# Optimization experiments

Hardware: AMD Instinct MI355X
Metric: run time of the kernel (lower is better)

The kernel has to match this reference:

```python
import jax, jax.numpy as jnp
import numpy as np

B, S, D, L, H = 8, 1024, 512, 6, 8
HD = D // H


def setup_inputs() -> dict:
    key = jax.random.key(0)
    sc = D ** -0.5
    inp = {
        "xr": jax.random.normal(jax.random.fold_in(key, 0), (B, S, D), jnp.float32),
        "xi": jax.random.normal(jax.random.fold_in(key, 1), (B, S, D), jnp.float32),
    }
    wnames = ["Wq_r", "Wq_i", "Wk_r", "Wk_i", "Wv_r", "Wv_i", "Wo_r", "Wo_i",
              "W1_r", "W1_i", "W2_r", "W2_i"]
    for i, n in enumerate(wnames):
        inp[n] = jax.random.normal(jax.random.fold_in(key, 10 + i), (L, D, D), jnp.float32) * sc
    for n in ["bq_r", "bq_i", "bk_r", "bk_i", "bv_r", "bv_i", "bo_r", "bo_i",
              "b1_r", "b1_i", "b2_r", "b2_i"]:
        inp[n] = jnp.zeros((L, D), jnp.float32)
    g0 = 1.0 / np.sqrt(2.0)  # standard complex-LN affine init
    for n in ["ln1_grr", "ln1_gii", "ln2_grr", "ln2_gii"]:
        inp[n] = jnp.full((L, D), g0, jnp.float32)
    for n in ["ln1_gri", "ln1_br", "ln1_bi", "ln2_gri", "ln2_br", "ln2_bi"]:
        inp[n] = jnp.zeros((L, D), jnp.float32)
    return inp


def clin(xr, xi, Wr, Wi, br, bi):
    # ComplexLinear: (xr + i xi)(Wr + i Wi)^T + (br + i bi)
    yr = xr @ Wr.T - xi @ Wi.T + br
    yi = xr @ Wi.T + xi @ Wr.T + bi
    return yr, yi


def cln(xr, xi, grr, gri, gii, br, bi, eps=1e-5):
    # Complex LayerNorm: 2x2 covariance whitening over the feature dim + affine
    mr = xr.mean(-1, keepdims=True)
    mi = xi.mean(-1, keepdims=True)
    cr, ci = xr - mr, xi - mi
    Vrr = (cr * cr).mean(-1, keepdims=True) + eps
    Vii = (ci * ci).mean(-1, keepdims=True) + eps
    Vri = (cr * ci).mean(-1, keepdims=True)
    s = jnp.sqrt(Vrr * Vii - Vri * Vri)
    t = jnp.sqrt(Vrr + Vii + 2.0 * s)
    st = s * t
    Wrr = (Vii + s) / st
    Wii = (Vrr + s) / st
    Wri = -Vri / st
    hr = Wrr * cr + Wri * ci
    hi = Wri * cr + Wii * ci
    return grr * hr + gri * hi + br, gri * hr + gii * hi + bi


def reference(xr, xi,
              Wq_r, Wq_i, bq_r, bq_i, Wk_r, Wk_i, bk_r, bk_i,
              Wv_r, Wv_i, bv_r, bv_i, Wo_r, Wo_i, bo_r, bo_i,
              W1_r, W1_i, b1_r, b1_i, W2_r, W2_i, b2_r, b2_i,
              ln1_grr, ln1_gri, ln1_gii, ln1_br, ln1_bi,
              ln2_grr, ln2_gri, ln2_gii, ln2_br, ln2_bi):
    b, s, d = xr.shape
    nl = Wq_r.shape[0]
    h = H
    hd = d // h
    scale = hd ** -0.5
    for l in range(nl):
        rr, ri = xr, xi
        qr, qi = clin(xr, xi, Wq_r[l], Wq_i[l], bq_r[l], bq_i[l])
        kr, ki = clin(xr, xi, Wk_r[l], Wk_i[l], bk_r[l], bk_i[l])
        vr, vi = clin(xr, xi, Wv_r[l], Wv_i[l], bv_r[l], bv_i[l])
        split = lambda a: a.reshape(b, s, h, hd)
        qr, qi, kr, ki, vr, vi = map(split, (qr, qi, kr, ki, vr, vi))
        # sm_variante='real': softmax over Re(q k^H) = qr.kr + qi.ki
        logits = (jnp.einsum('bqhd,bkhd->bhqk', qr, kr)
                  + jnp.einsum('bqhd,bkhd->bhqk', qi, ki)) * scale
        A = jax.nn.softmax(logits, axis=-1)  # real-valued attention weights
        o_r = jnp.einsum('bhqk,bkhd->bqhd', A, vr).reshape(b, s, d)
        o_i = jnp.einsum('bhqk,bkhd->bqhd', A, vi).reshape(b, s, d)
        o_r, o_i = clin(o_r, o_i, Wo_r[l], Wo_i[l], bo_r[l], bo_i[l])
        xr, xi = o_r + rr, o_i + ri
        xr, xi = cln(xr, xi, ln1_grr[l], ln1_gri[l], ln1_gii[l], ln1_br[l], ln1_bi[l])
        rr, ri = xr, xi
        hr, hi = clin(xr, xi, W1_r[l], W1_i[l], b1_r[l], b1_i[l])
        hr, hi = jax.nn.relu(hr), jax.nn.relu(hi)  # CReLU; dropout = identity (eval)
        hr, hi = clin(hr, hi, W2_r[l], W2_i[l], b2_r[l], b2_i[l])
        xr, xi = hr + rr, hi + ri
        xr, xi = cln(xr, xi, ln2_grr[l], ln2_gri[l], ln2_gii[l], ln2_br[l], ln2_bi[l])
    return jnp.stack([xr, xi])  # [2, B, S, D] (real, imag)
```

## Files before the change

kernel.cpp:

```cpp
#include <hip/hip_runtime.h>
#include <cstddef>
#include <cstdint>

constexpr int NB   = 8;
constexpr int SEQ  = 1024;
constexpr int DIM  = 512;
constexpr int NL   = 6;
constexpr int NH   = 8;
constexpr int HDIM = 64;
constexpr int ROWS = NB * SEQ;
constexpr size_t BSD = (size_t)ROWS * DIM;
constexpr int KHAT = 1024;

typedef __attribute__((ext_vector_type(8))) short bfrag;
typedef __attribute__((ext_vector_type(4))) float f32x4;
typedef __attribute__((ext_vector_type(4))) unsigned short us4;

__device__ __forceinline__ void f4a(const float4 v, float* a) {
    a[0] = v.x; a[1] = v.y; a[2] = v.z; a[3] = v.w;
}
__device__ __forceinline__ float4 a4f(const float* a) {
    float4 v; v.x = a[0]; v.y = a[1]; v.z = a[2]; v.w = a[3]; return v;
}
__device__ __forceinline__ unsigned short f2bf(float f) {
    union { float f; uint32_t u; } x{f};
    return (unsigned short)((x.u + 0x7fffu + ((x.u >> 16) & 1u)) >> 16);
}
__device__ __forceinline__ float bf2f(unsigned short u) {
    union { uint32_t u; float f; } x;
    x.u = (uint32_t)u << 16;
    return x.f;
}
__device__ __forceinline__ uint32_t cvtpk(float lo, float hi) {
    uint32_t r;
    asm("v_cvt_pk_bf16_f32 %0, %1, %2" : "=v"(r) : "v"(lo), "v"(hi));
    return r;
}
__device__ __forceinline__ void gload16(const unsigned short* g, void* l) {
    __builtin_amdgcn_global_load_lds(
        (const __attribute__((address_space(1))) void*)g,
        (__attribute__((address_space(3))) void*)l, 16, 0, 0);
}

constexpr float ATT_SC = 0.125f * 1.44269504f;

struct PrepArgs {
    const float* Wr[6]; const float* Wi[6];
    const float* br[6]; const float* bi[6];
};

__global__ __launch_bounds__(256)
void prep_kernel(PrepArgs a, unsigned short* __restrict__ Ball,
                 float* __restrict__ biasall, int layer)
{
    const int lin = blockIdx.y;
    const int nh_ = blockIdx.x;
    const float* Wr = a.Wr[lin] + (size_t)layer * DIM * DIM;
    const float* Wi = a.Wi[lin] + (size_t)layer * DIM * DIM;

    bool real; int n0;
    if (lin < 3) { const int dh = nh_ & 127; real = dh < 64; n0 = (nh_ >> 7) * 64 + (dh & 63); }
    else         { real = nh_ < 512; n0 = nh_ & 511; }

    const int t = threadIdx.x;
    const int kk = (t * 4) & 511;
    const bool fh = t < 128;
    const float* src;
    float sgn = 1.f;
    if (fh) src = real ? Wr : Wi;
    else { if (real) { src = Wi; sgn = -1.f; } else src = Wr; }

    float v[4];
    f4a(*(const float4*)(src + (size_t)n0 * 512 + kk), v);
    us4 o;
    #pragma unroll
    for (int j = 0; j < 4; ++j) o[j] = f2bf(sgn * v[j]);
    *(us4*)(Ball + (size_t)lin * KHAT * KHAT + (size_t)nh_ * KHAT + t * 4) = o;
    if (t == 0)
        biasall[lin * KHAT + nh_] = real ? a.br[lin][layer * DIM + n0]
                                         : a.bi[lin][layer * DIM + n0];
}

__global__ __launch_bounds__(256)
void gemm_qkv(const unsigned short* __restrict__ Xh,
              const unsigned short* __restrict__ Ball,
              const float* __restrict__ biasall,
              unsigned short* __restrict__ Qh,
              unsigned short* __restrict__ Kh,
              unsigned short* __restrict__ Vth)
{
    __shared__ __align__(16) unsigned short Asm[2][128 * 32];
    __shared__ __align__(16) unsigned short Bsm[2][128 * 32];

    const int t = threadIdx.x, lane = t & 63, w = t >> 6;
    const int wm = w >> 1, wn = w & 1;
    const int c = lane & 15, g = lane >> 4;

    int bid = blockIdx.y * 24 + blockIdx.x;
    bid = (bid & 7) * 192 + (bid >> 3);
    const int nblk = bid % 24, mblk = bid / 24;
    const int n0g = nblk * 128;
    const int m0 = mblk * 128;
    const int lin = n0g >> 10;
    const int n0 = n0g & 1023;
    const unsigned short* Bh = Ball + (size_t)lin * KHAT * KHAT;
    const float* bias = biasall + lin * KHAT;

    f32x4 acc[4][4];
    #pragma unroll
    for (int i = 0; i < 4; ++i)
        #pragma unroll
        for (int j = 0; j < 4; ++j) acc[i][j] = (f32x4){0.f, 0.f, 0.f, 0.f};

    const int srow = (w << 4) + (lane >> 2);
    const int scol = (lane & 3) * 8;
    const unsigned short* gA0 = Xh + (size_t)(m0 + srow) * KHAT + scol;
    const unsigned short* gA1 = Xh + (size_t)(m0 + 64 + srow) * KHAT + scol;
    const unsigned short* gB0 = Bh + (size_t)(n0 + srow) * KHAT + scol;
    const unsigned short* gB1 = Bh + (size_t)(n0 + 64 + srow) * KHAT + scol;
    char* aB0 = (char*)Asm[0] + (w << 10);
    char* aB1 = (char*)Asm[1] + (w << 10);
    char* bB0 = (char*)Bsm[0] + (w << 10);
    char* bB1 = (char*)Bsm[1] + (w << 10);

    for (int ks = 0; ks < 16; ++ks) {
        const int k0 = ks * 64;
        __syncthreads();
        gload16(gA0 + k0, aB0);
        gload16(gA1 + k0, aB0 + 4096);
        gload16(gB0 + k0, bB0);
        gload16(gB1 + k0, bB0 + 4096);
        gload16(gA0 + k0 + 32, aB1);
        gload16(gA1 + k0 + 32, aB1 + 4096);
        gload16(gB0 + k0 + 32, bB1);
        gload16(gB1 + k0 + 32, bB1 + 4096);
        __syncthreads();

        #pragma unroll
        for (int h = 0; h < 2; ++h) {
            bfrag af[4], bf2[4];
            #pragma unroll
            for (int mi = 0; mi < 4; ++mi)
                af[mi] = *(const bfrag*)(Asm[h] + (wm * 64 + mi * 16 + c) * 32 + g * 8);
            #pragma unroll
            for (int ni = 0; ni < 4; ++ni)
                bf2[ni] = *(const bfrag*)(Bsm[h] + (wn * 64 + ni * 16 + c) * 32 + g * 8);
            #pragma unroll
            for (int mi = 0; mi < 4; ++mi)
                #pragma unroll
                for (int ni = 0; ni < 4; ++ni)
                    acc[mi][ni] = __builtin_amdgcn_mfma_f32_16x16x32_bf16(
                        af[mi], bf2[ni], acc[mi][ni], 0, 0, 0);
        }
    }

    const int mbase = m0 + wm * 64;
    const int nbase = n0 + wn * 64;
    unsigned short* dqk = (lin == 0) ? Qh : Kh;
    #pragma unroll
    for (int mi = 0; mi < 4; ++mi) {
        #pragma unroll
        for (int ni = 0; ni < 4; ++ni) {
            const int n = nbase + ni * 16 + c;
            const float bv = bias[n];
            float v[4];
            #pragma unroll
            for (int r = 0; r < 4; ++r) {
                v[r] = acc[mi][ni][r] + bv;
                if (lin == 0) v[r] *= ATT_SC;
            }
            const int mrow = mbase + mi * 16 + g * 4;
            const int b = mrow >> 10, s = mrow & 1023;
            const int h = n >> 7, dh = n & 127;
            if (lin < 2) {
                const size_t a = ((size_t)(b * NH + h) * SEQ + s) * 128 + dh;
                #pragma unroll
                for (int r = 0; r < 4; ++r) dqk[a + (size_t)r * 128] = f2bf(v[r]);
            } else {
                const int ck = (s & 31) >> 2;
                const int sp = (s & ~31) | ((((ck & 3) << 1) | (ck >> 2)) << 2);
                const size_t a = ((size_t)(b * NH + h) * 128 + dh) * SEQ + sp;
                us4 o;
                #pragma unroll
                for (int r = 0; r < 4; ++r) o[r] = f2bf(v[r]);
                *(us4*)(Vth + a) = o;
            }
        }
    }
}

template <bool RELU>
__global__ __launch_bounds__(256)
void gemm_mfma(const unsigned short* __restrict__ Xh,
               const unsigned short* __restrict__ Bh,
               const float* __restrict__ bias,
               unsigned short* __restrict__ Yh)
{
    __shared__ __align__(16) unsigned short Asm[2][128 * 32];
    __shared__ __align__(16) unsigned short Bsm[2][128 * 32];

    const int t = threadIdx.x, lane = t & 63, w = t >> 6;
    const int wm = w >> 1, wn = w & 1;
    const int c = lane & 15, g = lane >> 4;

    int bid = blockIdx.y * 8 + blockIdx.x;
    bid = (bid & 7) * 64 + (bid >> 3);
    const int n0 = (bid & 7) * 128;
    const int m0 = (bid >> 3) * 128;

    f32x4 acc[4][4];
    #pragma unroll
    for (int i = 0; i < 4; ++i)
        #pragma unroll
        for (int j = 0; j < 4; ++j) acc[i][j] = (f32x4){0.f, 0.f, 0.f, 0.f};

    const int srow = (w << 4) + (lane >> 2);
    const int scol = (lane & 3) * 8;
    const unsigned short* gA0 = Xh + (size_t)(m0 + srow) * KHAT + scol;
    const unsigned short* gA1 = Xh + (size_t)(m0 + 64 + srow) * KHAT + scol;
    const unsigned short* gB0 = Bh + (size_t)(n0 + srow) * KHAT + scol;
    const unsigned short* gB1 = Bh + (size_t)(n0 + 64 + srow) * KHAT + scol;
    char* aB0 = (char*)Asm[0] + (w << 10);
    char* aB1 = (char*)Asm[1] + (w << 10);
    char* bB0 = (char*)Bsm[0] + (w << 10);
    char* bB1 = (char*)Bsm[1] + (w << 10);

    for (int ks = 0; ks < 16; ++ks) {
        const int k0 = ks * 64;
        __syncthreads();
        gload16(gA0 + k0, aB0);
        gload16(gA1 + k0, aB0 + 4096);
        gload16(gB0 + k0, bB0);
        gload16(gB1 + k0, bB0 + 4096);
        gload16(gA0 + k0 + 32, aB1);
        gload16(gA1 + k0 + 32, aB1 + 4096);
        gload16(gB0 + k0 + 32, bB1);
        gload16(gB1 + k0 + 32, bB1 + 4096);
        __syncthreads();

        #pragma unroll
        for (int h = 0; h < 2; ++h) {
            bfrag af[4], bf2[4];
            #pragma unroll
            for (int mi = 0; mi < 4; ++mi)
                af[mi] = *(const bfrag*)(Asm[h] + (wm * 64 + mi * 16 + c) * 32 + g * 8);
            #pragma unroll
            for (int ni = 0; ni < 4; ++ni)
                bf2[ni] = *(const bfrag*)(Bsm[h] + (wn * 64 + ni * 16 + c) * 32 + g * 8);
            #pragma unroll
            for (int mi = 0; mi < 4; ++mi)
                #pragma unroll
                for (int ni = 0; ni < 4; ++ni)
                    acc[mi][ni] = __builtin_amdgcn_mfma_f32_16x16x32_bf16(
                        af[mi], bf2[ni], acc[mi][ni], 0, 0, 0);
        }
    }

    const int mbase = m0 + wm * 64;
    const int nbase = n0 + wn * 64;
    #pragma unroll
    for (int mi = 0; mi < 4; ++mi) {
        #pragma unroll
        for (int ni = 0; ni < 4; ++ni) {
            const int n = nbase + ni * 16 + c;
            const float bv = bias[n];
            const int mrow = mbase + mi * 16 + g * 4;
            #pragma unroll
            for (int r = 0; r < 4; ++r) {
                float v = acc[mi][ni][r] + bv;
                if (RELU) v = fmaxf(v, 0.f);
                Yh[(size_t)(mrow + r) * KHAT + n] = f2bf(v);
            }
        }
    }
}

__global__ __launch_bounds__(256)
void attn_mfma(const unsigned short* __restrict__ Qh,
               const unsigned short* __restrict__ Kh,
               const unsigned short* __restrict__ Vth,
               unsigned short* __restrict__ Ah)
{
    __shared__ __align__(16) char smem[32768];
    char* Ksm = smem;
    char* Vsm = smem + 16384;
    const int t    = threadIdx.x;
    const int lane = t & 63;
    const int wv   = t >> 6;
    const int c    = lane & 15;
    const int g    = lane >> 4;

    int bid = blockIdx.x + 16 * blockIdx.y + 128 * blockIdx.z;
    bid = (bid & 7) * 128 + (bid >> 3);
    const int q0 = (bid & 15) * 64;
    const int bh = bid >> 4;
    const int hh = bh & 7, bb = bh >> 3;
    const size_t qkb = (size_t)bh * SEQ * 128;
    const size_t vtb = (size_t)bh * 128 * SEQ;

    constexpr float THR = 11.0f;

    bfrag qf[4];
    {
        const unsigned short* qp = Qh + qkb + (size_t)(q0 + wv * 16 + c) * 128 + g * 8;
        #pragma unroll
        for (int ks = 0; ks < 4; ++ks) qf[ks] = *(const bfrag*)(qp + ks * 32);
    }

    f32x4 oacc[8];
    #pragma unroll
    for (int i = 0; i < 8; ++i) oacc[i] = (f32x4){0.f, 0.f, 0.f, 0.f};
    float mrun = -1e30f, lrun = 0.f;

    const int kkey = t >> 2, kq = t & 3;
    const unsigned short* kgp = Kh + qkb + (size_t)kkey * 128 + kq * 32;
    const int vd = t >> 1, vh2 = t & 1;
    const unsigned short* vgp = Vth + vtb + (size_t)vd * SEQ + vh2 * 32;

    bfrag krg[4], vrg[4];
    #pragma unroll
    for (int j = 0; j < 4; ++j) krg[j] = *(const bfrag*)(kgp + j * 8);
    #pragma unroll
    for (int j = 0; j < 4; ++j) vrg[j] = *(const bfrag*)(vgp + j * 8);

    for (int k0 = 0; k0 < SEQ; k0 += 64) {
        __syncthreads();
        #pragma unroll
        for (int j = 0; j < 4; ++j) {
            const int boff = (kkey * 256 + (kq * 32 + j * 8) * 2) ^ ((kkey & 7) << 4);
            *(bfrag*)(Ksm + boff) = krg[j];
        }
        #pragma unroll
        for (int j = 0; j < 4; ++j) {
            const int boff = (vd * 128 + (vh2 * 32 + j * 8) * 2) ^ ((vd & 7) << 4);
            *(bfrag*)(Vsm + boff) = vrg[j];
        }
        __syncthreads();

        if (k0 + 64 < SEQ) {
            const int kn = k0 + 64;
            #pragma unroll
            for (int j = 0; j < 4; ++j) krg[j] = *(const bfrag*)(kgp + (size_t)kn * 128 + j * 8);
            #pragma unroll
            for (int j = 0; j < 4; ++j) vrg[j] = *(const bfrag*)(vgp + kn + j * 8);
        }

        f32x4 sa[4];
        #pragma unroll
        for (int nt = 0; nt < 4; ++nt) sa[nt] = (f32x4){0.f, 0.f, 0.f, 0.f};
        __builtin_amdgcn_s_setprio(1);
        #pragma unroll
        for (int nt = 0; nt < 4; ++nt) {
            const int key = nt * 16 + c;
            #pragma unroll
            for (int ks = 0; ks < 4; ++ks) {
                const int boff = (key * 256 + (ks * 32 + g * 8) * 2) ^ ((key & 7) << 4);
                const bfrag bk = *(const bfrag*)(Ksm + boff);
                sa[nt] = __builtin_amdgcn_mfma_f32_16x16x32_bf16(bk, qf[ks], sa[nt], 0, 0, 0);
            }
        }
        __builtin_amdgcn_s_setprio(0);

        float mloc = sa[0][0];
        #pragma unroll
        for (int nt = 0; nt < 4; ++nt)
            #pragma unroll
            for (int r = 0; r < 4; ++r) mloc = fmaxf(mloc, sa[nt][r]);
        if (__any(mloc > mrun + THR)) {
            float mt = mloc;
            mt = fmaxf(mt, __shfl_xor(mt, 16, 64));
            mt = fmaxf(mt, __shfl_xor(mt, 32, 64));
            const float mn = fmaxf(mrun, mt);
            const float fs = exp2f(mrun - mn);
            mrun = mn;
            lrun *= fs;
            #pragma unroll
            for (int i = 0; i < 8; ++i) {
                oacc[i][0] *= fs; oacc[i][1] *= fs; oacc[i][2] *= fs; oacc[i][3] *= fs;
            }
        }

        float p[4][4];
        float psum = 0.f;
        #pragma unroll
        for (int nt = 0; nt < 4; ++nt)
            #pragma unroll
            for (int r = 0; r < 4; ++r) {
                p[nt][r] = exp2f(sa[nt][r] - mrun);
                psum += p[nt][r];
            }
        psum += __shfl_xor(psum, 16, 64);
        psum += __shfl_xor(psum, 32, 64);
        lrun += psum;

        uint32_t pk0[4], pk1[4];
        #pragma unroll
        for (int nt = 0; nt < 4; ++nt) {
            pk0[nt] = cvtpk(p[nt][0], p[nt][1]);
            pk1[nt] = cvtpk(p[nt][2], p[nt][3]);
        }

        __builtin_amdgcn_s_setprio(1);
        #pragma unroll
        for (int k2 = 0; k2 < 2; ++k2) {
            union { uint32_t u[4]; bfrag f; } pb;
            pb.u[0] = pk0[2 * k2];
            pb.u[1] = pk1[2 * k2];
            pb.u[2] = pk0[2 * k2 + 1];
            pb.u[3] = pk1[2 * k2 + 1];
            const int kb2 = (k2 * 32 + g * 8) * 2;
            #pragma unroll
            for (int mtl = 0; mtl < 8; ++mtl) {
                const int d = mtl * 16 + c;
                const bfrag va = *(const bfrag*)(Vsm + ((d * 128 + kb2) ^ ((d & 7) << 4)));
                oacc[mtl] = __builtin_amdgcn_mfma_f32_16x16x32_bf16(va, pb.f, oacc[mtl], 0, 0, 0);
            }
        }
        __builtin_amdgcn_s_setprio(0);
    }

    {
        const float ic = 1.0f / lrun;
        #pragma unroll
        for (int i = 0; i < 8; ++i) {
            oacc[i][0] *= ic; oacc[i][1] *= ic; oacc[i][2] *= ic; oacc[i][3] *= ic;
        }
    }
    __syncthreads();
    float* Ox = (float*)(smem + wv * 8192);
    #pragma unroll
    for (int mtl = 0; mtl < 8; ++mtl)
        #pragma unroll
        for (int r = 0; r < 4; ++r)
            Ox[(mtl * 16 + 4 * g + r) * 16 + c] = oacc[mtl][r];
    asm volatile("s_waitcnt lgkmcnt(0)" ::: "memory");
    __builtin_amdgcn_sched_barrier(0);

    const int q = lane >> 2, qt = lane & 3;
    const int colbase = (qt >> 1) * 512 + hh * 64 + (qt & 1) * 32;
    const size_t rowm = (size_t)bb * SEQ + q0 + wv * 16 + q;
    unsigned short* dst = Ah + rowm * KHAT + colbase;
    #pragma unroll
    for (int j = 0; j < 8; ++j) {
        us4 o;
        #pragma unroll
        for (int e = 0; e < 4; ++e) o[e] = f2bf(Ox[(qt * 32 + j * 4 + e) * 16 + q]);
        *(us4*)(dst + j * 4) = o;
    }
}

__global__ __launch_bounds__(256)
void cln_kernel(const unsigned short* __restrict__ U,
                float* __restrict__ Xr, float* __restrict__ Xi,
                unsigned short* __restrict__ Xh,
                const float* __restrict__ Grr, const float* __restrict__ Gri,
                const float* __restrict__ Gii, const float* __restrict__ Bbr,
                const float* __restrict__ Bbi)
{
    const int lane = threadIdx.x & 63;
    const int row  = blockIdx.x * 4 + (threadIdx.x >> 6);
    const size_t off = (size_t)row * DIM;
    const int c0 = lane * 4;
    const int c1 = 256 + lane * 4;

    float xr[8], xi[8];
    {
        const unsigned short* up = U + (size_t)row * KHAT;
        us4 a0 = *(const us4*)(up + c0);
        us4 a1 = *(const us4*)(up + c1);
        us4 b0 = *(const us4*)(up + 512 + c0);
        us4 b1 = *(const us4*)(up + 512 + c1);
        float t0[4], t1[4];
        f4a(*(const float4*)&Xr[off + c0], t0);
        f4a(*(const float4*)&Xr[off + c1], t1);
        #pragma unroll
        for (int j = 0; j < 4; ++j) { xr[j] = bf2f(a0[j]) + t0[j]; xr[4 + j] = bf2f(a1[j]) + t1[j]; }
        f4a(*(const float4*)&Xi[off + c0], t0);
        f4a(*(const float4*)&Xi[off + c1], t1);
        #pragma unroll
        for (int j = 0; j < 4; ++j) { xi[j] = bf2f(b0[j]) + t0[j]; xi[4 + j] = bf2f(b1[j]) + t1[j]; }
    }

    float sr = 0.f, si = 0.f, srr = 0.f, sii = 0.f, sri = 0.f;
    #pragma unroll
    for (int j = 0; j < 8; ++j) {
        sr += xr[j]; si += xi[j];
        srr = fmaf(xr[j], xr[j], srr);
        sii = fmaf(xi[j], xi[j], sii);
        sri = fmaf(xr[j], xi[j], sri);
    }
    #pragma unroll
    for (int m = 32; m >= 1; m >>= 1) {
        sr  += __shfl_xor(sr,  m, 64);
        si  += __shfl_xor(si,  m, 64);
        srr += __shfl_xor(srr, m, 64);
        sii += __shfl_xor(sii, m, 64);
        sri += __shfl_xor(sri, m, 64);
    }

    const float inv_d = 1.0f / DIM;
    const float mr = sr * inv_d, mi = si * inv_d;
    const float Vrr = srr * inv_d - mr * mr + 1e-5f;
    const float Vii = sii * inv_d - mi * mi + 1e-5f;
    const float Vri = sri * inv_d - mr * mi;
    const float s  = sqrtf(Vrr * Vii - Vri * Vri);
    const float tt = sqrtf(Vrr + Vii + 2.0f * s);
    const float ist = 1.0f / (s * tt);
    const float Wrr = (Vii + s) * ist;
    const float Wii = (Vrr + s) * ist;
    const float Wri = -Vri * ist;

    #pragma unroll
    for (int half = 0; half < 2; ++half) {
        const int c = half ? c1 : c0;
        float grr[4], gri[4], gii[4], pbr[4], pbi[4];
        f4a(*(const float4*)&Grr[c], grr);
        f4a(*(const float4*)&Gri[c], gri);
        f4a(*(const float4*)&Gii[c], gii);
        f4a(*(const float4*)&Bbr[c], pbr);
        f4a(*(const float4*)&Bbi[c], pbi);
        float outr[4], outi[4];
        #pragma unroll
        for (int j = 0; j < 4; ++j) {
            const int idx = half * 4 + j;
            const float cr = xr[idx] - mr;
            const float ci = xi[idx] - mi;
            const float hr = Wrr * cr + Wri * ci;
            const float hi = Wri * cr + Wii * ci;
            outr[j] = fmaf(grr[j], hr, fmaf(gri[j], hi, pbr[j]));
            outi[j] = fmaf(gri[j], hr, fmaf(gii[j], hi, pbi[j]));
        }
        *(float4*)&Xr[off + c] = a4f(outr);
        *(float4*)&Xi[off + c] = a4f(outi);
        us4 hr_, hi_;
        #pragma unroll
        for (int j = 0; j < 4; ++j) { hr_[j] = f2bf(outr[j]); hi_[j] = f2bf(outi[j]); }
        *(us4*)(Xh + (size_t)row * KHAT + c)       = hr_;
        *(us4*)(Xh + (size_t)row * KHAT + 512 + c) = hi_;
    }
}

__global__ __launch_bounds__(256)
void init_cvt(const float* __restrict__ xr, const float* __restrict__ xi,
              float* __restrict__ outr, float* __restrict__ outi,
              unsigned short* __restrict__ Xh)
{
    const size_t i = ((size_t)blockIdx.x * 256 + threadIdx.x) * 4;
    float vr[4], vi[4];
    f4a(*(const float4*)(xr + i), vr);
    f4a(*(const float4*)(xi + i), vi);
    *(float4*)(outr + i) = a4f(vr);
    *(float4*)(outi + i) = a4f(vi);
    const size_t m = i >> 9;
    const int k = (int)(i & 511);
    us4 a, b;
    #pragma unroll
    for (int j = 0; j < 4; ++j) { a[j] = f2bf(vr[j]); b[j] = f2bf(vi[j]); }
    *(us4*)(Xh + m * KHAT + k)       = a;
    *(us4*)(Xh + m * KHAT + 512 + k) = b;
}

extern "C" void kernel_launch(void* const* d_in, const int* in_sizes, int n_in,
                              void* d_out, int out_size, void* d_ws, size_t ws_size,
                              hipStream_t stream) {
    (void)in_sizes; (void)n_in; (void)out_size; (void)ws_size;

    const float* in_xr = (const float*)d_in[0];
    const float* in_xi = (const float*)d_in[1];
    PrepArgs pa;
    pa.Wr[0] = (const float*)d_in[2];  pa.Wi[0] = (const float*)d_in[3];
    pa.Wr[1] = (const float*)d_in[4];  pa.Wi[1] = (const float*)d_in[5];
    pa.Wr[2] = (const float*)d_in[6];  pa.Wi[2] = (const float*)d_in[7];
    pa.Wr[3] = (const float*)d_in[8];  pa.Wi[3] = (const float*)d_in[9];
    pa.Wr[4] = (const float*)d_in[10]; pa.Wi[4] = (const float*)d_in[11];
    pa.Wr[5] = (const float*)d_in[12]; pa.Wi[5] = (const float*)d_in[13];
    pa.br[0] = (const float*)d_in[14]; pa.bi[0] = (const float*)d_in[15];
    pa.br[1] = (const float*)d_in[16]; pa.bi[1] = (const float*)d_in[17];
    pa.br[2] = (const float*)d_in[18]; pa.bi[2] = (const float*)d_in[19];
    pa.br[3] = (const float*)d_in[20]; pa.bi[3] = (const float*)d_in[21];
    pa.br[4] = (const float*)d_in[22]; pa.bi[4] = (const float*)d_in[23];
    pa.br[5] = (const float*)d_in[24]; pa.bi[5] = (const float*)d_in[25];
    const float* ln1_grr = (const float*)d_in[26];
    const float* ln1_gii = (const float*)d_in[27];
    const float* ln2_grr = (const float*)d_in[28];
    const float* ln2_gii = (const float*)d_in[29];
    const float* ln1_gri = (const float*)d_in[30];
    const float* ln1_br  = (const float*)d_in[31];
    const float* ln1_bi  = (const float*)d_in[32];
    const float* ln2_gri = (const float*)d_in[33];
    const float* ln2_br  = (const float*)d_in[34];
    const float* ln2_bi  = (const float*)d_in[35];

    float* outr = (float*)d_out;
    float* outi = outr + BSD;

    char* ws = (char*)d_ws;
    unsigned short* Xh  = (unsigned short*)(ws);
    unsigned short* Qh  = (unsigned short*)(ws + 16777216);
    unsigned short* Kh  = (unsigned short*)(ws + 2 * 16777216);
    unsigned short* Vth = (unsigned short*)(ws + 3 * 16777216);
    unsigned short* Ah  = (unsigned short*)(ws + 4 * 16777216);
    unsigned short* Ball = (unsigned short*)(ws + 5 * 16777216);
    float* biasall = (float*)(ws + 5 * 16777216 + 12582912);
    unsigned short* Uh = Kh;
    unsigned short* Hh = Qh;

    init_cvt<<<ROWS * DIM / 1024, 256, 0, stream>>>(in_xr, in_xi, outr, outi, Xh);

    const dim3 pgrid(KHAT, 6);
    const dim3 qgrid(24, ROWS / 128);
    const dim3 ggrid(KHAT / 128, ROWS / 128);
    const dim3 agrid(SEQ / 64, NH, NB);
    const int  lgrid = ROWS / 4;

    for (int l = 0; l < NL; ++l) {
        const size_t bo = (size_t)l * DIM;
        prep_kernel<<<pgrid, 256, 0, stream>>>(pa, Ball, biasall, l);

        unsigned short* Bo = Ball + (size_t)3 * KHAT * KHAT;
        unsigned short* B1 = Ball + (size_t)4 * KHAT * KHAT;
        unsigned short* B2 = Ball + (size_t)5 * KHAT * KHAT;

        gemm_qkv<<<qgrid, 256, 0, stream>>>(Xh, Ball, biasall, Qh, Kh, Vth);
        attn_mfma<<<agrid, 256, 0, stream>>>(Qh, Kh, Vth, Ah);
        gemm_mfma<false><<<ggrid, 256, 0, stream>>>(Ah, Bo, biasall + 3 * KHAT, Uh);
        cln_kernel<<<lgrid, 256, 0, stream>>>(Uh, outr, outi, Xh,
                                              ln1_grr + bo, ln1_gri + bo, ln1_gii + bo,
                                              ln1_br + bo, ln1_bi + bo);
        gemm_mfma<true><<<ggrid, 256, 0, stream>>>(Xh, B1, biasall + 4 * KHAT, Hh);
        gemm_mfma<false><<<ggrid, 256, 0, stream>>>(Hh, B2, biasall + 5 * KHAT, Uh);
        cln_kernel<<<lgrid, 256, 0, stream>>>(Uh, outr, outi, Xh,
                                              ln2_grr + bo, ln2_gri + bo, ln2_gii + bo,
                                              ln2_br + bo, ln2_bi + bo);
    }
}
```

Before: 1.493 ms.

## Process two query sub-tiles per wave in attention to reuse K/V fragments

```diff
diff --git a/kernel.cpp b/kernel.cpp
--- a/kernel.cpp
+++ b/kernel.cpp
@@ -290,27 +290,30 @@
     const int c    = lane & 15;
     const int g    = lane >> 4;
 
-    int bid = blockIdx.x + 16 * blockIdx.y + 128 * blockIdx.z;
-    bid = (bid & 7) * 128 + (bid >> 3);
-    const int q0 = (bid & 15) * 64;
-    const int bh = bid >> 4;
+    int bid = blockIdx.x + 8 * blockIdx.y + 64 * blockIdx.z;
+    bid = (bid & 7) * 64 + (bid >> 3);
+    const int q0 = (bid & 7) * 128;
+    const int bh = bid >> 3;
     const int hh = bh & 7, bb = bh >> 3;
     const size_t qkb = (size_t)bh * SEQ * 128;
     const size_t vtb = (size_t)bh * 128 * SEQ;
 
     constexpr float THR = 11.0f;
 
-    bfrag qf[4];
-    {
-        const unsigned short* qp = Qh + qkb + (size_t)(q0 + wv * 16 + c) * 128 + g * 8;
-        #pragma unroll
-        for (int ks = 0; ks < 4; ++ks) qf[ks] = *(const bfrag*)(qp + ks * 32);
-    }
-
-    f32x4 oacc[8];
-    #pragma unroll
-    for (int i = 0; i < 8; ++i) oacc[i] = (f32x4){0.f, 0.f, 0.f, 0.f};
-    float mrun = -1e30f, lrun = 0.f;
+    bfrag qf[2][4];
+    #pragma unroll
+    for (int u = 0; u < 2; ++u) {
+        const unsigned short* qp = Qh + qkb + (size_t)(q0 + wv * 32 + u * 16 + c) * 128 + g * 8;
+        #pragma unroll
+        for (int ks = 0; ks < 4; ++ks) qf[u][ks] = *(const bfrag*)(qp + ks * 32);
+    }
+
+    f32x4 oacc[2][8];
+    #pragma unroll
+    for (int u = 0; u < 2; ++u)
+        #pragma unroll
+        for (int i = 0; i < 8; ++i) oacc[u][i] = (f32x4){0.f, 0.f, 0.f, 0.f};
+    float mrun[2] = {-1e30f, -1e30f}, lrun[2] = {0.f, 0.f};
 
     const int kkey = t >> 2, kq = t & 3;
     const unsigned short* kgp = Kh + qkb + (size_t)kkey * 128 + kq * 32;
@@ -345,107 +348,121 @@
             for (int j = 0; j < 4; ++j) vrg[j] = *(const bfrag*)(vgp + kn + j * 8);
         }
 
-        f32x4 sa[4];
-        #pragma unroll
-        for (int nt = 0; nt < 4; ++nt) sa[nt] = (f32x4){0.f, 0.f, 0.f, 0.f};
+        f32x4 sa[2][4];
+        #pragma unroll
+        for (int u = 0; u < 2; ++u)
+            #pragma unroll
+            for (int nt = 0; nt < 4; ++nt) sa[u][nt] = (f32x4){0.f, 0.f, 0.f, 0.f};
         __builtin_amdgcn_s_setprio(1);
         #pragma unroll
         for (int nt = 0; nt < 4; ++nt) {
             const int key = nt * 16 + c;
+            bfrag kf[4];
             #pragma unroll
             for (int ks = 0; ks < 4; ++ks) {
                 const int boff = (key * 256 + (ks * 32 + g * 8) * 2) ^ ((key & 7) << 4);
-                const bfrag bk = *(const bfrag*)(Ksm + boff);
-                sa[nt] = __builtin_amdgcn_mfma_f32_16x16x32_bf16(bk, qf[ks], sa[nt], 0, 0, 0);
+                kf[ks] = *(const bfrag*)(Ksm + boff);
             }
+            #pragma unroll
+            for (int u = 0; u < 2; ++u)
+                #pragma unroll
+                for (int ks = 0; ks < 4; ++ks)
+                    sa[u][nt] = __builtin_amdgcn_mfma_f32_16x16x32_bf16(kf[ks], qf[u][ks], sa[u][nt], 0, 0, 0);
         }
         __builtin_amdgcn_s_setprio(0);
 
-        float mloc = sa[0][0];
-        #pragma unroll
-        for (int nt = 0; nt < 4; ++nt)
-            #pragma unroll
-            for (int r = 0; r < 4; ++r) mloc = fmaxf(mloc, sa[nt][r]);
-        if (__any(mloc > mrun + THR)) {
-            float mt = mloc;
-            mt = fmaxf(mt, __shfl_xor(mt, 16, 64));
-            mt = fmaxf(mt, __shfl_xor(mt, 32, 64));
-            const float mn = fmaxf(mrun, mt);
-            const float fs = exp2f(mrun - mn);
-            mrun = mn;
-            lrun *= fs;
-            #pragma unroll
-            for (int i = 0; i < 8; ++i) {
-                oacc[i][0] *= fs; oacc[i][1] *= fs; oacc[i][2] *= fs; oacc[i][3] *= fs;
+        uint32_t pk0[2][4], pk1[2][4];
+        #pragma unroll
+        for (int u = 0; u < 2; ++u) {
+            float mloc = sa[u][0][0];
+            #pragma unroll
+            for (int nt = 0; nt < 4; ++nt)
+                #pragma unroll
+                for (int r = 0; r < 4; ++r) mloc = fmaxf(mloc, sa[u][nt][r]);
+            if (__any(mloc > mrun[u] + THR)) {
+                float mt = mloc;
+                mt = fmaxf(mt, __shfl_xor(mt, 16, 64));
+                mt = fmaxf(mt, __shfl_xor(mt, 32, 64));
+                const float mn = fmaxf(mrun[u], mt);
+                const float fs = exp2f(mrun[u] - mn);
+                mrun[u] = mn;
+                lrun[u] *= fs;
+                #pragma unroll
+                for (int i = 0; i < 8; ++i) {
+                    oacc[u][i][0] *= fs; oacc[u][i][1] *= fs;
+                    oacc[u][i][2] *= fs; oacc[u][i][3] *= fs;
+                }
             }
-        }
-
-        float p[4][4];
-        float psum = 0.f;
-        #pragma unroll
-        for (int nt = 0; nt < 4; ++nt)
-            #pragma unroll
-            for (int r = 0; r < 4; ++r) {
-                p[nt][r] = exp2f(sa[nt][r] - mrun);
-                psum += p[nt][r];
+            float ps = 0.f;
+            #pragma unroll
+            for (int nt = 0; nt < 4; ++nt) {
+                float p0 = exp2f(sa[u][nt][0] - mrun[u]);
+                float p1 = exp2f(sa[u][nt][1] - mrun[u]);
+                float p2 = exp2f(sa[u][nt][2] - mrun[u]);
+                float p3 = exp2f(sa[u][nt][3] - mrun[u]);
+                ps += (p0 + p1) + (p2 + p3);
+                pk0[u][nt] = cvtpk(p0, p1);
+                pk1[u][nt] = cvtpk(p2, p3);
             }
-        psum += __shfl_xor(psum, 16, 64);
-        psum += __shfl_xor(psum, 32, 64);
-        lrun += psum;
-
-        uint32_t pk0[4], pk1[4];
-        #pragma unroll
-        for (int nt = 0; nt < 4; ++nt) {
-            pk0[nt] = cvtpk(p[nt][0], p[nt][1]);
-            pk1[nt] = cvtpk(p[nt][2], p[nt][3]);
+            ps += __shfl_xor(ps, 16, 64);
+            ps += __shfl_xor(ps, 32, 64);
+            lrun[u] += ps;
         }
 
         __builtin_amdgcn_s_setprio(1);
         #pragma unroll
         for (int k2 = 0; k2 < 2; ++k2) {
-            union { uint32_t u[4]; bfrag f; } pb;
-            pb.u[0] = pk0[2 * k2];
-            pb.u[1] = pk1[2 * k2];
-            pb.u[2] = pk0[2 * k2 + 1];
-            pb.u[3] = pk1[2 * k2 + 1];
+            union { uint32_t u[4]; bfrag f; } pb0, pb1;
+            pb0.u[0] = pk0[0][2 * k2]; pb0.u[1] = pk1[0][2 * k2];
+            pb0.u[2] = pk0[0][2 * k2 + 1]; pb0.u[3] = pk1[0][2 * k2 + 1];
+            pb1.u[0] = pk0[1][2 * k2]; pb1.u[1] = pk1[1][2 * k2];
+            pb1.u[2] = pk0[1][2 * k2 + 1]; pb1.u[3] = pk1[1][2 * k2 + 1];
             const int kb2 = (k2 * 32 + g * 8) * 2;
             #pragma unroll
             for (int mtl = 0; mtl < 8; ++mtl) {
                 const int d = mtl * 16 + c;
                 const bfrag va = *(const bfrag*)(Vsm + ((d * 128 + kb2) ^ ((d & 7) << 4)));
-                oacc[mtl] = __builtin_amdgcn_mfma_f32_16x16x32_bf16(va, pb.f, oacc[mtl], 0, 0, 0);
+                oacc[0][mtl] = __builtin_amdgcn_mfma_f32_16x16x32_bf16(va, pb0.f, oacc[0][mtl], 0, 0, 0);
+                oacc[1][mtl] = __builtin_amdgcn_mfma_f32_16x16x32_bf16(va, pb1.f, oacc[1][mtl], 0, 0, 0);
             }
         }
         __builtin_amdgcn_s_setprio(0);
     }
 
-    {
-        const float ic = 1.0f / lrun;
+    #pragma unroll
+    for (int u = 0; u < 2; ++u) {
+        const float ic = 1.0f / lrun[u];
         #pragma unroll
         for (int i = 0; i < 8; ++i) {
-            oacc[i][0] *= ic; oacc[i][1] *= ic; oacc[i][2] *= ic; oacc[i][3] *= ic;
+            oacc[u][i][0] *= ic; oacc[u][i][1] *= ic;
+            oacc[u][i][2] *= ic; oacc[u][i][3] *= ic;
         }
     }
     __syncthreads();
     float* Ox = (float*)(smem + wv * 8192);
-    #pragma unroll
-    for (int mtl = 0; mtl < 8; ++mtl)
-        #pragma unroll
-        for (int r = 0; r < 4; ++r)
-            Ox[(mtl * 16 + 4 * g + r) * 16 + c] = oacc[mtl][r];
-    asm volatile("s_waitcnt lgkmcnt(0)" ::: "memory");
-    __builtin_amdgcn_sched_barrier(0);
-
     const int q = lane >> 2, qt = lane & 3;
     const int colbase = (qt >> 1) * 512 + hh * 64 + (qt & 1) * 32;
-    const size_t rowm = (size_t)bb * SEQ + q0 + wv * 16 + q;
-    unsigned short* dst = Ah + rowm * KHAT + colbase;
-    #pragma unroll
-    for (int j = 0; j < 8; ++j) {
-        us4 o;
-        #pragma unroll
-        for (int e = 0; e < 4; ++e) o[e] = f2bf(Ox[(qt * 32 + j * 4 + e) * 16 + q]);
-        *(us4*)(dst + j * 4) = o;
+    #pragma unroll
+    for (int u = 0; u < 2; ++u) {
+        #pragma unroll
+        for (int mtl = 0; mtl < 8; ++mtl)
+            #pragma unroll
+            for (int r = 0; r < 4; ++r)
+                Ox[(mtl * 16 + 4 * g + r) * 16 + c] = oacc[u][mtl][r];
+        asm volatile("s_waitcnt lgkmcnt(0)" ::: "memory");
+        __builtin_amdgcn_sched_barrier(0);
+
+        const size_t rowm = (size_t)bb * SEQ + q0 + wv * 32 + u * 16 + q;
+        unsigned short* dst = Ah + rowm * KHAT + colbase;
+        #pragma unroll
+        for (int j = 0; j < 8; ++j) {
+            us4 o;
+            #pragma unroll
+            for (int e = 0; e < 4; ++e) o[e] = f2bf(Ox[(qt * 32 + j * 4 + e) * 16 + q]);
+            *(us4*)(dst + j * 4) = o;
+        }
+        asm volatile("s_waitcnt lgkmcnt(0)" ::: "memory");
+        __builtin_amdgcn_sched_barrier(0);
     }
 }
 
@@ -610,7 +627,7 @@
     const dim3 pgrid(KHAT, 6);
     const dim3 qgrid(24, ROWS / 128);
     const dim3 ggrid(KHAT / 128, ROWS / 128);
-    const dim3 agrid(SEQ / 64, NH, NB);
+    const dim3 agrid(SEQ / 128, NH, NB);
     const int  lgrid = ROWS / 4;
 
     for (int l = 0; l < NL; ++l) {
```

New measurement: 1.498 ms. Within noise of the previous version (+0.3%).
